# Kernel optimization log

Measured on AMD Instinct MI355X. Metric: run time of the kernel, lower is better.

The kernel has to match this reference:

```python
import jax, jax.numpy as jnp
import numpy as np

B = 8
IN_FEATURES = 8192
OUT_FEATURES = 8192


def setup_inputs() -> dict:
    key = jax.random.key(0)
    k_x, k_w, k_b = jax.random.split(key, 3)
    x = jax.random.normal(k_x, (B, IN_FEATURES), dtype=jnp.float32)
    # kaiming-uniform-like init for weight [out, in]
    bound_w = np.sqrt(6.0 / IN_FEATURES)  # approx kaiming_uniform with a=sqrt(5)
    weight = jax.random.uniform(k_w, (OUT_FEATURES, IN_FEATURES), dtype=jnp.float32,
                                minval=-bound_w, maxval=bound_w)
    bound_b = 1.0 / np.sqrt(IN_FEATURES)
    bias = jax.random.uniform(k_b, (OUT_FEATURES,), dtype=jnp.float32,
                              minval=-bound_b, maxval=bound_b)
    return {"input": x, "weight": weight, "bias": bias}


def reference(input, weight, bias):
    # Ternary (sign) quantize both operands, then GEMV per batch row:
    # out[b, o] = sum_i sign(x[b, i]) * sign(W[o, i])  (+ bias)
    x_t = jnp.sign(input)            # [B, in] in {-1, 0, +1}
    w_t = jnp.sign(weight)           # [out, in] in {-1, 0, +1}
    out = jnp.einsum('bi,oi->bo', x_t, w_t)  # [B, out]
    return out + bias
```

## Files before the change

kernel.cpp:

```cpp
#include <hip/hip_runtime.h>
#include <stdint.h>

#define IN_F 8192
#define OUT_F 8192
#define BATCH 8
#define XPW (BATCH * 4 * 64)

typedef unsigned int u32x4 __attribute__((ext_vector_type(4)));

__global__ __launch_bounds__(256) void pack_sign_perm(
    const u32x4* __restrict__ x, uint32_t* __restrict__ xp) {
  const int t = blockIdx.x * 256 + threadIdx.x;
  const int b = t >> 8;
  const int m = (t >> 6) & 3;
  const int l = t & 63;
  const u32x4* base = x + (b * IN_F + m * 2048 + l * 4) / 4;
  uint32_t w = 0;
#pragma unroll
  for (int i = 0; i < 8; ++i) {
    u32x4 u = base[i * 64];
    uint32_t nib = (u.x >> 31) | ((u.y >> 31) << 1) |
                   ((u.z >> 31) << 2) | ((u.w >> 31) << 3);
    w |= nib << (4 * i);
  }
  xp[t] = w;
}

__global__ __launch_bounds__(256) void ternary_gemv2(
    const u32x4* __restrict__ W, const uint32_t* __restrict__ xp,
    const float* __restrict__ bias, float* __restrict__ out) {
  __shared__ uint32_t xl[XPW];
  for (int i = threadIdx.x; i < XPW; i += 256) xl[i] = xp[i];
  __syncthreads();

  const int warp = threadIdx.x >> 6;
  const int lane = threadIdx.x & 63;
  const int row = blockIdx.x * 4 + warp;
  const u32x4* wrow = W + (size_t)row * (IN_F / 4);

  int cnt[BATCH] = {0, 0, 0, 0, 0, 0, 0, 0};

#pragma unroll
  for (int m = 0; m < 4; ++m) {
    u32x4 u[8];
#pragma unroll
    for (int i = 0; i < 8; ++i)
      u[i] = __builtin_nontemporal_load(&wrow[m * 512 + i * 64 + lane]);

    uint32_t wn = 0;
#pragma unroll
    for (int i = 0; i < 8; ++i) {
      uint32_t nib = (u[i].x >> 31) | ((u[i].y >> 31) << 1) |
                     ((u[i].z >> 31) << 2) | ((u[i].w >> 31) << 3);
      wn |= nib << (4 * i);
    }

#pragma unroll
    for (int b = 0; b < BATCH; ++b)
      cnt[b] += __popc(wn ^ xl[(b * 4 + m) * 64 + lane]);
  }

#pragma unroll
  for (int b = 0; b < BATCH; ++b) {
#pragma unroll
    for (int off = 32; off > 0; off >>= 1)
      cnt[b] += __shfl_down(cnt[b], off);
  }

  if (lane == 0) {
    const float bv = bias[row];
#pragma unroll
    for (int b = 0; b < BATCH; ++b)
      out[(size_t)b * OUT_F + row] = (float)(IN_F - 2 * cnt[b]) + bv;
  }
}

extern "C" void kernel_launch(void* const* d_in, const int* in_sizes, int n_in,
                              void* d_out, int out_size, void* d_ws, size_t ws_size,
                              hipStream_t stream) {
  const u32x4* x = (const u32x4*)d_in[0];
  const u32x4* W = (const u32x4*)d_in[1];
  const float* bias = (const float*)d_in[2];
  float* out = (float*)d_out;
  uint32_t* xp = (uint32_t*)d_ws;

  pack_sign_perm<<<XPW / 256, 256, 0, stream>>>(x, xp);
  ternary_gemv2<<<OUT_F / 4, 256, 0, stream>>>(W, xp, bias, out);
}
```

Baseline: 51.00 us.

## Fuse sign-packing of activations into the ternary GEMV kernel

Removes the separate pack kernel and has every block pack the signs of the full activation matrix (256 KB read per block) into shared memory itself, after first issuing its own weight loads. This drops one kernel launch and the global round trip through the workspace. In exchange, each of the 2048 blocks rereads all of x, which adds a lot of L2 traffic and per-block latency next to the HBM-bound weight stream.

```diff
diff --git a/kernel.cpp b/kernel.cpp
--- a/kernel.cpp
+++ b/kernel.cpp
@@ -4,60 +4,59 @@
 #define IN_F 8192
 #define OUT_F 8192
 #define BATCH 8
-#define XPW (BATCH * 4 * 64)
+#define XPW 2048
 
 typedef unsigned int u32x4 __attribute__((ext_vector_type(4)));
 
-__global__ __launch_bounds__(256) void pack_sign_perm(
-    const u32x4* __restrict__ x, uint32_t* __restrict__ xp) {
-  const int t = blockIdx.x * 256 + threadIdx.x;
-  const int b = t >> 8;
-  const int m = (t >> 6) & 3;
-  const int l = t & 63;
-  const u32x4* base = x + (b * IN_F + m * 2048 + l * 4) / 4;
-  uint32_t w = 0;
-#pragma unroll
-  for (int i = 0; i < 8; ++i) {
-    u32x4 u = base[i * 64];
-    uint32_t nib = (u.x >> 31) | ((u.y >> 31) << 1) |
-                   ((u.z >> 31) << 2) | ((u.w >> 31) << 3);
-    w |= nib << (4 * i);
-  }
-  xp[t] = w;
-}
-
-__global__ __launch_bounds__(256) void ternary_gemv2(
-    const u32x4* __restrict__ W, const uint32_t* __restrict__ xp,
+__global__ __launch_bounds__(256) void ternary_fused(
+    const u32x4* __restrict__ W, const u32x4* __restrict__ x,
     const float* __restrict__ bias, float* __restrict__ out) {
   __shared__ uint32_t xl[XPW];
-  for (int i = threadIdx.x; i < XPW; i += 256) xl[i] = xp[i];
-  __syncthreads();
 
   const int warp = threadIdx.x >> 6;
   const int lane = threadIdx.x & 63;
   const int row = blockIdx.x * 4 + warp;
   const u32x4* wrow = W + (size_t)row * (IN_F / 4);
 
-  int cnt[BATCH] = {0, 0, 0, 0, 0, 0, 0, 0};
-
+  uint32_t wn[4];
 #pragma unroll
   for (int m = 0; m < 4; ++m) {
     u32x4 u[8];
 #pragma unroll
     for (int i = 0; i < 8; ++i)
       u[i] = __builtin_nontemporal_load(&wrow[m * 512 + i * 64 + lane]);
-
-    uint32_t wn = 0;
+    uint32_t v = 0;
 #pragma unroll
     for (int i = 0; i < 8; ++i) {
       uint32_t nib = (u[i].x >> 31) | ((u[i].y >> 31) << 1) |
                      ((u[i].z >> 31) << 2) | ((u[i].w >> 31) << 3);
-      wn |= nib << (4 * i);
+      v |= nib << (4 * i);
     }
+    wn[m] = v;
+  }
 
 #pragma unroll
+  for (int j = 0; j < 8; ++j) {
+    const int bm = j * 4 + warp;
+    const u32x4* base = x + bm * 512 + lane;
+    uint32_t v = 0;
+#pragma unroll
+    for (int i = 0; i < 8; ++i) {
+      u32x4 u = base[i * 64];
+      uint32_t nib = (u.x >> 31) | ((u.y >> 31) << 1) |
+                     ((u.z >> 31) << 2) | ((u.w >> 31) << 3);
+      v |= nib << (4 * i);
+    }
+    xl[bm * 64 + lane] = v;
+  }
+  __syncthreads();
+
+  int cnt[BATCH] = {0, 0, 0, 0, 0, 0, 0, 0};
+#pragma unroll
+  for (int m = 0; m < 4; ++m) {
+#pragma unroll
     for (int b = 0; b < BATCH; ++b)
-      cnt[b] += __popc(wn ^ xl[(b * 4 + m) * 64 + lane]);
+      cnt[b] += __popc(wn[m] ^ xl[(b * 4 + m) * 64 + lane]);
   }
 
 #pragma unroll
@@ -82,8 +81,7 @@
   const u32x4* W = (const u32x4*)d_in[1];
   const float* bias = (const float*)d_in[2];
   float* out = (float*)d_out;
-  uint32_t* xp = (uint32_t*)d_ws;
+  (void)d_ws; (void)ws_size;
 
-  pack_sign_perm<<<XPW / 256, 256, 0, stream>>>(x, xp);
-  ternary_gemv2<<<OUT_F / 4, 256, 0, stream>>>(W, xp, bias, out);
+  ternary_fused<<<OUT_F / 4, 256, 0, stream>>>(W, x, bias, out);
 }
```

After: 59.91 us. 17.5% more time.
